# Optimization experiments

Hardware: AMD Instinct MI355X
Metric: run time of the kernel (lower is better)

## Reference

```python
import jax, jax.numpy as jnp
import numpy as np

B, S1, S2 = 1024, 25, 10          # batch, hop-1 fanout, hop-2 fanout
N, D, H, C = 100000, 256, 128, 64  # n_node, in_dim, per-branch out_dim, n_class


def setup_inputs() -> dict:
    key = jax.random.key(0)
    ks = jax.random.split(key, 10)
    rn = lambda k, shape: jax.random.normal(k, shape, dtype=jnp.float32) * 0.05
    return {
        "ids0": jax.random.randint(ks[0], (B,), 0, N),
        "ids1": jax.random.randint(ks[1], (B * S1,), 0, N),
        "ids2": jax.random.randint(ks[2], (B * S1 * S2,), 0, N),
        "features": jax.random.normal(ks[3], (N, D), dtype=jnp.float32),
        # aggregator layer 1 (in D, out 2H after concat)
        "Wx1": rn(ks[4], (D, H)), "bx1": jnp.zeros((H,), jnp.float32),
        "Wn1": rn(ks[5], (D, H)), "bn1": jnp.zeros((H,), jnp.float32),
        # aggregator layer 2 (in 2H, out 2H)
        "Wx2": rn(ks[6], (2 * H, H)), "bx2": jnp.zeros((H,), jnp.float32),
        "Wn2": rn(ks[7], (2 * H, H)), "bn2": jnp.zeros((H,), jnp.float32),
        # final linear head
        "Wfc": rn(ks[8], (2 * H, C)), "bfc": jnp.zeros((C,), jnp.float32),
    }


def _mean_agg(x, neibs, Wx, bx, Wn, bn, act):
    # neibs: [x_rows * fanout, d] -> mean over fanout, then concat of two linears
    n = neibs.reshape(x.shape[0], -1, neibs.shape[-1]).mean(axis=1)
    out = jnp.concatenate([x @ Wx + bx, n @ Wn + bn], axis=-1)
    return act(out)


def reference(ids0, ids1, ids2, features,
              Wx1, bx1, Wn1, bn1, Wx2, bx2, Wn2, bn2, Wfc, bfc):
    # hop-wise feature gathers (identity prep)
    h0 = features[ids0]   # [B, D]
    h1 = features[ids1]   # [B*S1, D]
    h2 = features[ids2]   # [B*S1*S2, D]
    # layer 1 aggregation (relu), applied to consecutive hop pairs
    g0 = _mean_agg(h0, h1, Wx1, bx1, Wn1, bn1, jax.nn.relu)   # [B, 2H]
    g1 = _mean_agg(h1, h2, Wx1, bx1, Wn1, bn1, jax.nn.relu)   # [B*S1, 2H]
    # layer 2 aggregation (identity activation on last layer)
    f0 = _mean_agg(g0, g1, Wx2, bx2, Wn2, bn2, lambda v: v)   # [B, 2H]
    return f0 @ Wfc + bfc  # [B, C]
```

## Files before the change

### kernel.cpp

```cpp
#include <hip/hip_runtime.h>

#define DD 256
#define HH 128
#define CC 64
#define BB 1024
#define SS1 25
#define SS2 10
#define NN 100000

typedef __attribute__((ext_vector_type(8))) short bf16x8;
typedef __attribute__((ext_vector_type(4))) float f32x4;

__device__ inline unsigned short f2b(float x) {
    union { float f; unsigned u; } v; v.f = x;
    unsigned r = (v.u + 0x7fffu + ((v.u >> 16) & 1u)) >> 16;
    return (unsigned short)r;
}
__device__ inline float b2f(unsigned u16) {
    union { unsigned u; float f; } v; v.u = u16 << 16;
    return v.f;
}

__global__ __launch_bounds__(256)
void prep_w(const float* __restrict__ Wx, const float* __restrict__ Wn,
            unsigned short* __restrict__ Wsw) {
    const int t    = blockIdx.x * 256 + threadIdx.x;
    const int lane = t & 63;
    const int frag = t >> 6;
    const int kc = frag >> 4, nt = frag & 15;
    const int quad = lane >> 4, lr = lane & 15;
    unsigned short v[8];
#pragma unroll
    for (int j = 0; j < 8; ++j) {
        int k = kc * 32 + quad * 8 + j;
        int n = nt * 16 + lr;
        float w = (n < HH) ? Wx[k * HH + n] : Wn[k * HH + (n - HH)];
        v[j] = f2b(w);
    }
    ((uint4*)Wsw)[t] = *(uint4*)v;
}

#define PQ_GRID   1536
#define PQ_TILES  (NN / 32)
#define PQ_TASKS  (PQ_TILES * 2)
#define AS 264
#define OS 132

__global__ __launch_bounds__(256, 3)
void pq_gemm(const float* __restrict__ feat,
             const unsigned short* __restrict__ Wsw,
             unsigned short* __restrict__ PQb) {
    __shared__ unsigned short sA[32 * AS];
    __shared__ unsigned short sO[32 * OS];
    const int t    = threadIdx.x;
    const int w    = t >> 6, lane = t & 63;
    const int quad = lane >> 4, lr = lane & 15;
    const int by   = blockIdx.x & 1;

    bf16x8 B[8][2];
#pragma unroll
    for (int kc = 0; kc < 8; ++kc)
#pragma unroll
        for (int j = 0; j < 2; ++j) {
            int nt = by * 8 + w * 2 + j;
            B[kc][j] = *(const bf16x8*)&Wsw[((kc * 16 + nt) * 64 + lane) * 8];
        }

    const int srow = t >> 5, sc = t & 31;

    float4 v[8];
    long task = blockIdx.x;
    {
        const float* fb = feat + (task >> 1) * 32 * DD + sc * 8;
#pragma unroll
        for (int i = 0; i < 4; ++i) {
            const float4* src = (const float4*)(fb + (long)(i * 8 + srow) * DD);
            v[2 * i]     = src[0];
            v[2 * i + 1] = src[1];
        }
    }

#pragma unroll 1
    while (true) {
        const long tile = task >> 1;
#pragma unroll
        for (int i = 0; i < 4; ++i) {
            int row = i * 8 + srow;
            float4 a = v[2 * i], b = v[2 * i + 1];
            unsigned short w8[8] = { f2b(a.x), f2b(a.y), f2b(a.z), f2b(a.w),
                                     f2b(b.x), f2b(b.y), f2b(b.z), f2b(b.w) };
            *(uint4*)&sA[row * AS + sc * 8] = *(uint4*)w8;
        }
        long tn = task + PQ_GRID;
        if (tn < PQ_TASKS) {
            const float* fn = feat + (tn >> 1) * 32 * DD + sc * 8;
#pragma unroll
            for (int i = 0; i < 4; ++i) {
                const float4* src = (const float4*)(fn + (long)(i * 8 + srow) * DD);
                v[2 * i]     = src[0];
                v[2 * i + 1] = src[1];
            }
        }
        asm volatile("s_waitcnt lgkmcnt(0)" ::: "memory");
        __builtin_amdgcn_s_barrier();

        f32x4 acc[2][2] = {};
#pragma unroll
        for (int kc = 0; kc < 8; ++kc) {
            bf16x8 a0 = *(const bf16x8*)&sA[(lr)      * AS + kc * 32 + quad * 8];
            bf16x8 a1 = *(const bf16x8*)&sA[(16 + lr) * AS + kc * 32 + quad * 8];
#pragma unroll
            for (int j = 0; j < 2; ++j) {
                acc[0][j] = __builtin_amdgcn_mfma_f32_16x16x32_bf16(a0, B[kc][j], acc[0][j], 0, 0, 0);
                acc[1][j] = __builtin_amdgcn_mfma_f32_16x16x32_bf16(a1, B[kc][j], acc[1][j], 0, 0, 0);
            }
        }
#pragma unroll
        for (int rt = 0; rt < 2; ++rt)
#pragma unroll
            for (int j = 0; j < 2; ++j) {
                int col = (w * 2 + j) * 16 + lr;
#pragma unroll
                for (int r = 0; r < 4; ++r)
                    sO[(rt * 16 + quad * 4 + r) * OS + col] = f2b(acc[rt][j][r]);
            }
        asm volatile("s_waitcnt lgkmcnt(0)" ::: "memory");
        __builtin_amdgcn_s_barrier();

#pragma unroll
        for (int i = 0; i < 2; ++i) {
            int id  = i * 256 + t;
            int row = id >> 4, ch = id & 15;
            uint4 d = *(uint4*)&sO[row * OS + ch * 8];
            *(uint4*)&PQb[(tile * 32 + row) * DD + by * HH + ch * 8] = d;
        }
        task = tn;
        if (task >= PQ_TASKS) break;
    }
}

__global__ __launch_bounds__(512)
void megatail(const unsigned short* __restrict__ PQb,
              const int* __restrict__ ids0, const int* __restrict__ ids1,
              const int* __restrict__ ids2,
              const float* __restrict__ bx1, const float* __restrict__ bn1,
              const float* __restrict__ Wx2, const float* __restrict__ bx2,
              const float* __restrict__ Wn2, const float* __restrict__ bn2,
              const float* __restrict__ Wfc, const float* __restrict__ bfc,
              float* __restrict__ out) {
    __shared__ float sred[8][3 * HH];
    __shared__ float g0L[DD];
    __shared__ float gmL[DD];
    __shared__ float FP[2][DD];
    __shared__ float FL[DD];
    __shared__ float sp[8][CC];
    const int i    = blockIdx.x;
    const int t    = threadIdx.x;
    const int wv   = t >> 6, lane = t & 63;
    const int l16  = lane & 15;
    const int slot = wv * 4 + (lane >> 4);
    const int c0   = l16 * 8;

    float xs[8], ns[8], g0n[8];
#pragma unroll
    for (int k = 0; k < 8; ++k) { xs[k] = 0.f; ns[k] = 0.f; g0n[k] = 0.f; }

    if (slot < SS1) {
        const int row = i * SS1 + slot;
        const long xr = (long)ids1[row];
        uint4 xv  = *(const uint4*)&PQb[xr * DD + c0];
        uint4 nv0 = *(const uint4*)&PQb[xr * DD + HH + c0];
        int myid = ids2[row * SS2 + (l16 % SS2)];
        float pa[8];
#pragma unroll
        for (int k = 0; k < 8; ++k) pa[k] = 0.f;
#pragma unroll
        for (int j = 0; j < SS2; ++j) {
            long nr = (long)__shfl(myid, (lane & 48) + j);
            uint4 nv = *(const uint4*)&PQb[nr * DD + HH + c0];
            pa[0] += b2f(nv.x & 0xffff); pa[1] += b2f(nv.x >> 16);
            pa[2] += b2f(nv.y & 0xffff); pa[3] += b2f(nv.y >> 16);
            pa[4] += b2f(nv.z & 0xffff); pa[5] += b2f(nv.z >> 16);
            pa[6] += b2f(nv.w & 0xffff); pa[7] += b2f(nv.w >> 16);
        }
        const float4 bxa = *(const float4*)&bx1[c0];
        const float4 bxb = *(const float4*)&bx1[c0 + 4];
        const float4 bna = *(const float4*)&bn1[c0];
        const float4 bnb = *(const float4*)&bn1[c0 + 4];
        constexpr float inv2 = 1.f / SS2;
        xs[0] = fmaxf(b2f(xv.x & 0xffff) + bxa.x, 0.f);
        xs[1] = fmaxf(b2f(xv.x >> 16)    + bxa.y, 0.f);
        xs[2] = fmaxf(b2f(xv.y & 0xffff) + bxa.z, 0.f);
        xs[3] = fmaxf(b2f(xv.y >> 16)    + bxa.w, 0.f);
        xs[4] = fmaxf(b2f(xv.z & 0xffff) + bxb.x, 0.f);
        xs[5] = fmaxf(b2f(xv.z >> 16)    + bxb.y, 0.f);
        xs[6] = fmaxf(b2f(xv.w & 0xffff) + bxb.z, 0.f);
        xs[7] = fmaxf(b2f(xv.w >> 16)    + bxb.w, 0.f);
        ns[0] = fmaxf(pa[0] * inv2 + bna.x, 0.f);
        ns[1] = fmaxf(pa[1] * inv2 + bna.y, 0.f);
        ns[2] = fmaxf(pa[2] * inv2 + bna.z, 0.f);
        ns[3] = fmaxf(pa[3] * inv2 + bna.w, 0.f);
        ns[4] = fmaxf(pa[4] * inv2 + bnb.x, 0.f);
        ns[5] = fmaxf(pa[5] * inv2 + bnb.y, 0.f);
        ns[6] = fmaxf(pa[6] * inv2 + bnb.z, 0.f);
        ns[7] = fmaxf(pa[7] * inv2 + bnb.w, 0.f);
        g0n[0] = b2f(nv0.x & 0xffff); g0n[1] = b2f(nv0.x >> 16);
        g0n[2] = b2f(nv0.y & 0xffff); g0n[3] = b2f(nv0.y >> 16);
        g0n[4] = b2f(nv0.z & 0xffff); g0n[5] = b2f(nv0.z >> 16);
        g0n[6] = b2f(nv0.w & 0xffff); g0n[7] = b2f(nv0.w >> 16);
    }

#pragma unroll
    for (int k = 0; k < 8; ++k) {
        xs[k]  += __shfl_xor(xs[k], 16);  xs[k]  += __shfl_xor(xs[k], 32);
        ns[k]  += __shfl_xor(ns[k], 16);  ns[k]  += __shfl_xor(ns[k], 32);
        g0n[k] += __shfl_xor(g0n[k], 16); g0n[k] += __shfl_xor(g0n[k], 32);
    }
    if (lane < 16) {
        *(float4*)&sred[wv][c0]              = make_float4(xs[0], xs[1], xs[2], xs[3]);
        *(float4*)&sred[wv][c0 + 4]          = make_float4(xs[4], xs[5], xs[6], xs[7]);
        *(float4*)&sred[wv][HH + c0]         = make_float4(ns[0], ns[1], ns[2], ns[3]);
        *(float4*)&sred[wv][HH + c0 + 4]     = make_float4(ns[4], ns[5], ns[6], ns[7]);
        *(float4*)&sred[wv][2 * HH + c0]     = make_float4(g0n[0], g0n[1], g0n[2], g0n[3]);
        *(float4*)&sred[wv][2 * HH + c0 + 4] = make_float4(g0n[4], g0n[5], g0n[6], g0n[7]);
    }
    __syncthreads();

    if (t < 384) {
        float r = 0.f;
#pragma unroll
        for (int k = 0; k < 8; ++k) r += sred[k][t];
        if (t < 256) {
            gmL[t] = r * (1.f / SS1);
        } else {
            const int c = t - 256;
            g0L[HH + c] = fmaxf(r * (1.f / SS1) + bn1[c], 0.f);
        }
    } else {
        const int c = t - 384;
        unsigned short u = PQb[(long)ids0[i] * DD + c];
        g0L[c] = fmaxf(b2f(u) + bx1[c], 0.f);
    }
    __syncthreads();

    {
        const int c = t & 255, h = t >> 8;
        const bool xhalf = (c < HH);
        const float* __restrict__ W    = xhalf ? Wx2 : Wn2;
        const float* __restrict__ srcL = xhalf ? g0L : gmL;
        const int cc = c & (HH - 1);
        float fa = 0.f;
#pragma unroll 8
        for (int k = h * 128; k < h * 128 + 128; ++k) fa += srcL[k] * W[k * HH + cc];
        FP[h][c] = fa;
    }
    __syncthreads();
    if (t < 256)
        FL[t] = FP[0][t] + FP[1][t] + ((t < HH) ? bx2[t] : bn2[t - HH]);
    __syncthreads();

    {
        const int col = t & (CC - 1), q = t >> 6;
        float p = 0.f;
#pragma unroll 8
        for (int k = q * 32; k < q * 32 + 32; ++k) p += FL[k] * Wfc[k * CC + col];
        sp[q][col] = p;
    }
    __syncthreads();
    if (t < CC) {
        float r = bfc[t];
#pragma unroll
        for (int q = 0; q < 8; ++q) r += sp[q][t];
        out[(long)i * CC + t] = r;
    }
}

extern "C" void kernel_launch(void* const* d_in, const int* in_sizes, int n_in,
                              void* d_out, int out_size, void* d_ws, size_t ws_size,
                              hipStream_t stream) {
    const int*   ids0 = (const int*)d_in[0];
    const int*   ids1 = (const int*)d_in[1];
    const int*   ids2 = (const int*)d_in[2];
    const float* feat = (const float*)d_in[3];
    const float* Wx1  = (const float*)d_in[4];
    const float* bx1  = (const float*)d_in[5];
    const float* Wn1  = (const float*)d_in[6];
    const float* bn1  = (const float*)d_in[7];
    const float* Wx2  = (const float*)d_in[8];
    const float* bx2  = (const float*)d_in[9];
    const float* Wn2  = (const float*)d_in[10];
    const float* bn2  = (const float*)d_in[11];
    const float* Wfc  = (const float*)d_in[12];
    const float* bfc  = (const float*)d_in[13];
    float* out = (float*)d_out;

    unsigned short* PQb = (unsigned short*)d_ws;
    unsigned short* Wsw = PQb + (long)NN * DD;

    prep_w<<<32, 256, 0, stream>>>(Wx1, Wn1, Wsw);
    pq_gemm<<<PQ_GRID, 256, 0, stream>>>(feat, Wsw, PQb);
    megatail<<<BB, 512, 0, stream>>>(PQb, ids0, ids1, ids2, bx1, bn1,
                                     Wx2, bx2, Wn2, bn2, Wfc, bfc, out);
}
```

Before: 221.7 us.

## Split megatail into gather, batched layer-2 GEMM, and head kernels

The per-row tail kernel is split into three kernels. One gathers and mean-reduces neighbour rows into global g0/gm buffers. A layer-2 GEMM then processes 8 rows per block so each weight load is reused across 4 rows per thread, and a separate head kernel applies the final linear layer. Previously every one of the 1024 blocks reread the full Wx2/Wn2/Wfc matrices for a single row. The change adds two kernel launches and global round-trips for the intermediates, and moves the workspace offsets.

New measurement: 258.9 us. +16.7%, slower.

```diff
diff --git a/kernel.cpp b/kernel.cpp
--- a/kernel.cpp
+++ b/kernel.cpp
@@ -140,20 +140,12 @@
 }
 
 __global__ __launch_bounds__(512)
-void megatail(const unsigned short* __restrict__ PQb,
-              const int* __restrict__ ids0, const int* __restrict__ ids1,
-              const int* __restrict__ ids2,
-              const float* __restrict__ bx1, const float* __restrict__ bn1,
-              const float* __restrict__ Wx2, const float* __restrict__ bx2,
-              const float* __restrict__ Wn2, const float* __restrict__ bn2,
-              const float* __restrict__ Wfc, const float* __restrict__ bfc,
-              float* __restrict__ out) {
+void gather_gm(const unsigned short* __restrict__ PQb,
+               const int* __restrict__ ids0, const int* __restrict__ ids1,
+               const int* __restrict__ ids2,
+               const float* __restrict__ bx1, const float* __restrict__ bn1,
+               float* __restrict__ g0, float* __restrict__ gm) {
     __shared__ float sred[8][3 * HH];
-    __shared__ float g0L[DD];
-    __shared__ float gmL[DD];
-    __shared__ float FP[2][DD];
-    __shared__ float FL[DD];
-    __shared__ float sp[8][CC];
     const int i    = blockIdx.x;
     const int t    = threadIdx.x;
     const int wv   = t >> 6, lane = t & 63;
@@ -231,48 +223,87 @@
 #pragma unroll
         for (int k = 0; k < 8; ++k) r += sred[k][t];
         if (t < 256) {
-            gmL[t] = r * (1.f / SS1);
+            gm[(long)i * DD + t] = r * (1.f / SS1);
         } else {
             const int c = t - 256;
-            g0L[HH + c] = fmaxf(r * (1.f / SS1) + bn1[c], 0.f);
+            g0[(long)i * DD + HH + c] = fmaxf(r * (1.f / SS1) + bn1[c], 0.f);
         }
     } else {
         const int c = t - 384;
         unsigned short u = PQb[(long)ids0[i] * DD + c];
-        g0L[c] = fmaxf(b2f(u) + bx1[c], 0.f);
+        g0[(long)i * DD + c] = fmaxf(b2f(u) + bx1[c], 0.f);
+    }
+}
+
+__global__ __launch_bounds__(256)
+void agg2(const float* __restrict__ g0, const float* __restrict__ gm,
+          const float* __restrict__ Wx, const float* __restrict__ bx,
+          const float* __restrict__ Wn, const float* __restrict__ bn,
+          float* __restrict__ f0) {
+    constexpr int RT = 8;
+    __shared__ float A[RT][DD];
+    const int r0 = blockIdx.x * RT;
+    const int by = blockIdx.y;
+    const int t  = threadIdx.x;
+    const float* __restrict__ src = by ? gm : g0;
+    const float* __restrict__ W   = by ? Wn : Wx;
+    const float* __restrict__ bb  = by ? bn : bx;
+
+#pragma unroll
+    for (int i = 0; i < 2; ++i) {
+        int id = i * 256 + t;
+        int r = id >> 6, c4 = (id & 63) * 4;
+        *(float4*)&A[r][c4] = *(const float4*)(src + (long)(r0 + r) * DD + c4);
     }
     __syncthreads();
 
-    {
-        const int c = t & 255, h = t >> 8;
-        const bool xhalf = (c < HH);
-        const float* __restrict__ W    = xhalf ? Wx2 : Wn2;
-        const float* __restrict__ srcL = xhalf ? g0L : gmL;
-        const int cc = c & (HH - 1);
-        float fa = 0.f;
-#pragma unroll 8
-        for (int k = h * 128; k < h * 128 + 128; ++k) fa += srcL[k] * W[k * HH + cc];
-        FP[h][c] = fa;
+    const int c  = t & 127;
+    const int rh = t >> 7;
+    float acc[4];
+#pragma unroll
+    for (int r = 0; r < 4; ++r) acc[r] = 0.f;
+#pragma unroll 4
+    for (int k = 0; k < DD; ++k) {
+        float wv = W[k * HH + c];
+#pragma unroll
+        for (int r = 0; r < 4; ++r) acc[r] += A[rh * 4 + r][k] * wv;
+    }
+    const float bias = bb[c];
+#pragma unroll
+    for (int r = 0; r < 4; ++r)
+        f0[(long)(r0 + rh * 4 + r) * DD + by * HH + c] = acc[r] + bias;
+}
+
+__global__ __launch_bounds__(256)
+void head_kernel(const float* __restrict__ f0, const float* __restrict__ Wfc,
+                 const float* __restrict__ bfc, float* __restrict__ out) {
+    constexpr int RT = 8;
+    __shared__ float aX[RT][DD];
+    const int r0 = blockIdx.x * RT;
+    const int t  = threadIdx.x;
+
+#pragma unroll
+    for (int i = 0; i < 2; ++i) {
+        int id = i * 256 + t;
+        int r = id >> 6, c4 = (id & 63) * 4;
+        *(float4*)&aX[r][c4] = *(const float4*)(f0 + (long)(r0 + r) * DD + c4);
     }
     __syncthreads();
-    if (t < 256)
-        FL[t] = FP[0][t] + FP[1][t] + ((t < HH) ? bx2[t] : bn2[t - HH]);
-    __syncthreads();
-
-    {
-        const int col = t & (CC - 1), q = t >> 6;
-        float p = 0.f;
-#pragma unroll 8
-        for (int k = q * 32; k < q * 32 + 32; ++k) p += FL[k] * Wfc[k * CC + col];
-        sp[q][col] = p;
-    }
-    __syncthreads();
-    if (t < CC) {
-        float r = bfc[t];
-#pragma unroll
-        for (int q = 0; q < 8; ++q) r += sp[q][t];
-        out[(long)i * CC + t] = r;
-    }
+
+    const int c  = t & (CC - 1);
+    const int rg = t >> 6;
+    float acc[2];
+    acc[0] = 0.f; acc[1] = 0.f;
+#pragma unroll 4
+    for (int k = 0; k < DD; ++k) {
+        float wv = Wfc[k * CC + c];
+#pragma unroll
+        for (int r = 0; r < 2; ++r) acc[r] += aX[rg * 2 + r][k] * wv;
+    }
+    const float bias = bfc[c];
+#pragma unroll
+    for (int r = 0; r < 2; ++r)
+        out[(long)(r0 + rg * 2 + r) * CC + c] = acc[r] + bias;
 }
 
 extern "C" void kernel_launch(void* const* d_in, const int* in_sizes, int n_in,
@@ -294,11 +325,16 @@
     const float* bfc  = (const float*)d_in[13];
     float* out = (float*)d_out;
 
-    unsigned short* PQb = (unsigned short*)d_ws;
+    float* wsf = (float*)d_ws;
+    float* g0 = wsf;  wsf += (long)BB * DD;
+    float* gm = wsf;  wsf += (long)BB * DD;
+    float* f0 = wsf;  wsf += (long)BB * DD;
+    unsigned short* PQb = (unsigned short*)wsf;
     unsigned short* Wsw = PQb + (long)NN * DD;
 
     prep_w<<<32, 256, 0, stream>>>(Wx1, Wn1, Wsw);
     pq_gemm<<<PQ_GRID, 256, 0, stream>>>(feat, Wsw, PQb);
-    megatail<<<BB, 512, 0, stream>>>(PQb, ids0, ids1, ids2, bx1, bn1,
-                                     Wx2, bx2, Wn2, bn2, Wfc, bfc, out);
-}
+    gather_gm<<<BB, 512, 0, stream>>>(PQb, ids0, ids1, ids2, bx1, bn1, g0, gm);
+    agg2<<<dim3(BB / 8, 2), 256, 0, stream>>>(g0, gm, Wx2, bx2, Wn2, bn2, f0);
+    head_kernel<<<BB / 8, 256, 0, stream>>>(f0, Wfc, bfc, out);
+}
```
